# Performance work log

Measured on AMD Instinct MI355X. Metric: run time of the kernel, lower is better.

## Reference

```python
import jax, jax.numpy as jnp
import numpy as np

B, C, H, W = 4, 1024, 14, 14
L = 80          # num labels / graph nodes
WD = 300        # word embedding dim
INTER = 1024    # semantic intermediary dim
OUT = 2048      # output_dim
TIME_STEP = 3


def setup_inputs() -> dict:
    key = jax.random.key(0)
    ks = jax.random.split(key, 24)
    s = 0.02  # weight scale to keep gates/tanh in sane range
    return {
        "img_feature_map": jax.random.normal(ks[0], (B, C, H, W), jnp.float32),
        "word_embedding": jax.random.normal(ks[1], (L, WD), jnp.float32),
        "adjacency": jax.random.uniform(ks[2], (L, L), jnp.float32) / L,
        "fc1_w": jax.random.normal(ks[3], (INTER, C), jnp.float32) * s,
        "fc2_w": jax.random.normal(ks[4], (INTER, WD), jnp.float32) * s,
        "fc3_w": jax.random.normal(ks[5], (INTER, INTER), jnp.float32) * s,
        "fc3_b": jnp.zeros((INTER,), jnp.float32),
        "fca_w": jax.random.normal(ks[6], (1, INTER), jnp.float32) * s,
        "fca_b": jnp.zeros((1,), jnp.float32),
        "w3": jax.random.normal(ks[7], (C, 2 * C), jnp.float32) * s,
        "b3": jnp.zeros((C,), jnp.float32),
        "u3": jax.random.normal(ks[8], (C, C), jnp.float32) * s,
        "u3b": jnp.zeros((C,), jnp.float32),
        "w4": jax.random.normal(ks[9], (C, 2 * C), jnp.float32) * s,
        "b4": jnp.zeros((C,), jnp.float32),
        "w5": jax.random.normal(ks[10], (C, 2 * C), jnp.float32) * s,
        "b5": jnp.zeros((C,), jnp.float32),
        "u5": jax.random.normal(ks[11], (C, C), jnp.float32) * s,
        "u5b": jnp.zeros((C,), jnp.float32),
        "fco_w": jax.random.normal(ks[12], (OUT, 2 * C), jnp.float32) * s,
        "fco_b": jnp.zeros((OUT,), jnp.float32),
    }


def _semantic(fmap, word_emb, fc1_w, fc2_w, fc3_w, fc3_b, fca_w, fca_b):
    # Faithful to torch: view(-1, C) on a contiguous (B,C,H,W) tensor is a raw
    # row-major reinterpret (NOT a BHWC transpose). jnp.reshape matches.
    b, c, h, w = fmap.shape
    x = fmap.reshape(-1, c)                                   # (B*H*W, C)
    f_wh = x @ fc1_w.T                                        # (N, INTER)
    f_wd = word_emb @ fc2_w.T                                 # (L, INTER)
    lb = jnp.tanh(f_wh[:, None, :] * f_wd[None, :, :])        # (N, L, INTER)
    lb = lb @ fc3_w.T + fc3_b                                 # (N, L, INTER)
    coeff = lb @ fca_w.T + fca_b                              # (N, L, 1)
    coeff = coeff.reshape(b, L, h * w)                        # torch .view semantics
    coeff = jax.nn.softmax(coeff, axis=2)
    coeff = coeff.reshape(b, h, w, L)
    fmap_bhwc = fmap.reshape(b, h, w, c)                      # raw reinterpret, as torch
    return jnp.einsum('bhwl,bhwc->blc', coeff, fmap_bhwc)     # (B, L, C)


def _ggnn(nodes, adj, w3, b3, u3, u3b, w4, b4, w5, b5, u5, u5b):
    for _ in range(TIME_STEP):
        a = jnp.einsum('nm,bmd->bnd', adj, nodes)             # in == out matrix
        av = jnp.concatenate([a, a], axis=-1)                 # (B, L, 2C)
        u3x = nodes @ u3.T + u3b
        z = jax.nn.sigmoid(av @ w3.T + b3 + u3x)
        r = jax.nn.sigmoid(av @ w4.T + b4 + u3x)              # torch bug: reuses fc_eq3_u
        hcand = jnp.tanh(av @ w5.T + b5 + (r * nodes) @ u5.T + u5b)
        nodes = (1.0 - z) * nodes + z * hcand
    return nodes


def reference(img_feature_map, word_embedding, adjacency,
              fc1_w, fc2_w, fc3_w, fc3_b, fca_w, fca_b,
              w3, b3, u3, u3b, w4, b4, w5, b5, u5, u5b,
              fco_w, fco_b):
    g = _semantic(img_feature_map, word_embedding,
                  fc1_w, fc2_w, fc3_w, fc3_b, fca_w, fca_b)   # (B, L, C)
    nodes = _ggnn(g, adjacency, w3, b3, u3, u3b, w4, b4, w5, b5, u5, u5b)
    feat = jnp.concatenate([nodes, g], axis=-1)               # (B, L, 2C)
    out = jnp.tanh(feat @ fco_w.T + fco_b)                    # (B, L, OUT)
    return out
```

## Files before the change

kernel.cpp:

```cpp
#include <hip/hip_runtime.h>
#include <hip/hip_bf16.h>

#define LL 80
#define NPIX 784
#define PBATCH 15680

#define DI __device__ __forceinline__

typedef short s8v __attribute__((ext_vector_type(8)));
typedef short short4v __attribute__((ext_vector_type(4)));
typedef float f32x4 __attribute__((ext_vector_type(4)));

DI float b2f(__hip_bfloat16 x) { return __bfloat162float(x); }
DI float s2f(short h) { return __uint_as_float(((unsigned int)(unsigned short)h) << 16); }

DI short f2b(float x) {
    unsigned int b = __float_as_uint(x);
    b += 0x7fffu + ((b >> 16) & 1u);
    return (short)(b >> 16);
}

template <int F> DI float LD(const void* p, int i) {
    if (F) return ((const float*)p)[i];
    return b2f(((const __hip_bfloat16*)p)[i]);
}

DI float fast_tanh(float x) {
    float e = __expf(2.0f * x);
    return 1.0f - 2.0f / (e + 1.0f);
}
DI float fast_sigmoid(float x) { return 1.0f / (1.0f + __expf(-x)); }

__global__ __launch_bounds__(256) void detect_dtype(const void* probe, int n, int* flag) {
    __shared__ int bad;
    if (threadIdx.x == 0) bad = 0;
    __syncthreads();
    int c = 0;
    for (int i = threadIdx.x; i < n; i += 256) {
        float v = b2f(((const __hip_bfloat16*)probe)[i]);
        if (!(fabsf(v) < 1000.0f)) c++;
    }
    if (c) atomicAdd(&bad, c);
    __syncthreads();
    if (threadIdx.x == 0) *flag = (bad > 8) ? 1 : 0;
}

DI void cvt_part(int f, const void* src, short* __restrict__ dst, int blk, int n) {
    int i0 = (blk * 256 + threadIdx.x) * 4;
    if (i0 >= n) return;
    if (f) {
        float4 v = *(const float4*)((const float*)src + i0);
        short4v o = { f2b(v.x), f2b(v.y), f2b(v.z), f2b(v.w) };
        *(short4v*)(dst + i0) = o;
    } else {
        *(short4v*)(dst + i0) = *(const short4v*)((const short*)src + i0);
    }
}

DI void cvt_pad(int f, const void* src, short* __restrict__ dst, int blk, int n) {
    int i0 = (blk * 256 + threadIdx.x) * 4;
    if (i0 >= n) return;
    int row = i0 / 320;
    int k = i0 - row * 320;
    short4v o = {0, 0, 0, 0};
    if (k < 300) {
        if (f) {
            float4 v = *(const float4*)((const float*)src + row * 300 + k);
            o.x = f2b(v.x); o.y = f2b(v.y); o.z = f2b(v.z); o.w = f2b(v.w);
        } else {
            o = *(const short4v*)((const short*)src + row * 300 + k);
        }
    }
    *(short4v*)(dst + i0) = o;
}

DI void wcat_part(int f, const void* w3, const void* w4, const void* w5, const void* u3,
                  short* __restrict__ wcat, int blk) {
    int i0 = (blk * 256 + threadIdx.x) * 4;
    int nr = i0 >> 10, k = i0 & 1023;
    int j = nr >> 10, r = nr & 1023;
    const void* W = (j == 0) ? w3 : (j == 1) ? w4 : (j == 2) ? w5 : u3;
    float4 v;
    if (j < 3) {
        if (f) {
            float4 x = *(const float4*)((const float*)W + r * 2048 + k);
            float4 y = *(const float4*)((const float*)W + r * 2048 + 1024 + k);
            v.x = x.x + y.x; v.y = x.y + y.y; v.z = x.z + y.z; v.w = x.w + y.w;
        } else {
            const short* Ws = (const short*)W;
            short4v x = *(const short4v*)(Ws + r * 2048 + k);
            short4v y = *(const short4v*)(Ws + r * 2048 + 1024 + k);
            v.x = s2f(x.x) + s2f(y.x); v.y = s2f(x.y) + s2f(y.y);
            v.z = s2f(x.z) + s2f(y.z); v.w = s2f(x.w) + s2f(y.w);
        }
    } else {
        if (f) v = *(const float4*)((const float*)W + r * 1024 + k);
        else {
            short4v x = *(const short4v*)((const short*)W + r * 1024 + k);
            v.x = s2f(x.x); v.y = s2f(x.y); v.z = s2f(x.z); v.w = s2f(x.w);
        }
    }
    short4v o = { f2b(v.x), f2b(v.y), f2b(v.z), f2b(v.w) };
    *(short4v*)(wcat + i0) = o;
}

template <int F>
DI void prep_upart(const void* fc3_w, const void* fca_w,
                   float* __restrict__ u_part, int blk) {
    int kseg = blk >> 4, jseg = blk & 15;
    int k = kseg * 256 + threadIdx.x;
    int j0 = jseg * 64;
    float acc = 0.f;
    for (int j = j0; j < j0 + 64; j++)
        acc += LD<F>(fca_w, j) * LD<F>(fc3_w, j * 1024 + k);
    u_part[jseg * 1024 + k] = acc;
}

template <int F>
DI void prep_c0(const void* fc3_b, const void* fca_w, const void* fca_b,
                float* c0, float* red) {
    float acc = 0.f;
    for (int j = threadIdx.x; j < 1024; j += 256)
        acc += LD<F>(fc3_b, j) * LD<F>(fca_w, j);
    red[threadIdx.x] = acc;
    __syncthreads();
    for (int s = 128; s > 0; s >>= 1) {
        if (threadIdx.x < s) red[threadIdx.x] += red[threadIdx.x + s];
        __syncthreads();
    }
    if (threadIdx.x == 0) *c0 = red[0] + LD<F>(fca_b, 0);
}

__global__ __launch_bounds__(256) void mega_prep(
    const int* flag,
    const void* fmap, const void* fc1_w, const void* u5w,
    const void* w3, const void* w4, const void* w5, const void* u3,
    const void* fc3_w, const void* fc3_b, const void* fca_w, const void* fca_b,
    const void* word, const void* fc2_w,
    short* fmap_b, short* fc1w_b, short* u5w_b, short* wcat_b,
    short* word_b, short* fc2w_b,
    float* u_part, float* c0) {
    __shared__ float red[256];
    int f = *flag;
    int bid = blockIdx.x;
    if      (bid < 784)  cvt_part(f, fmap,  fmap_b, bid,        802816);
    else if (bid < 1808) cvt_part(f, fc1_w, fc1w_b, bid - 784,  1048576);
    else if (bid < 2832) cvt_part(f, u5w,   u5w_b,  bid - 1808, 1048576);
    else if (bid < 6928) wcat_part(f, w3, w4, w5, u3, wcat_b, bid - 2832);
    else if (bid < 6992) {
        if (f) prep_upart<1>(fc3_w, fca_w, u_part, bid - 6928);
        else   prep_upart<0>(fc3_w, fca_w, u_part, bid - 6928);
    } else if (bid == 6992) {
        if (f) prep_c0<1>(fc3_b, fca_w, fca_b, c0, red);
        else   prep_c0<0>(fc3_b, fca_w, fca_b, c0, red);
    }
    else if (bid < 7018) cvt_pad(f, word,  word_b, bid - 6993, 25600);
    else                 cvt_pad(f, fc2_w, fc2w_b, bid - 7018, 327680);
}

__global__ __launch_bounds__(256) void cvt_k(const int* flag, const void* src,
                                             short* __restrict__ dst, int n) {
    cvt_part(*flag, src, dst, blockIdx.x, n);
}

DI void mcore_b(const short* __restrict__ A, int lda,
                const short* __restrict__ B, int ldb,
                float* __restrict__ C, int ldc,
                int M, int kb, int ke, int m0, int n0) {
    __shared__ short As[4][64][8];
    __shared__ short Ws[4][64][8];
    const int tid = threadIdx.x;
    const int wv = tid >> 6, lane = tid & 63;
    const int mA = tid & 63, qA = tid >> 6;
    f32x4 acc[4] = {};

    for (int k0 = kb; k0 < ke; k0 += 32) {
        s8v va = {0,0,0,0,0,0,0,0};
        int gm = m0 + mA;
        if (gm < M) va = *(const s8v*)(A + gm * lda + k0 + 8 * qA);
        *(s8v*)&As[mA >> 4][(mA & 15) | (qA << 4)][0] = va;
        s8v vb = *(const s8v*)(B + (n0 + mA) * ldb + k0 + 8 * qA);
        *(s8v*)&Ws[mA >> 4][(mA & 15) | (qA << 4)][0] = vb;
        __syncthreads();
        s8v af = *(const s8v*)&As[wv][lane][0];
#pragma unroll
        for (int nf = 0; nf < 4; nf++) {
            s8v bf = *(const s8v*)&Ws[nf][lane][0];
            acc[nf] = __builtin_amdgcn_mfma_f32_16x16x32_bf16(af, bf, acc[nf], 0, 0, 0);
        }
        __syncthreads();
    }

    const int q = lane >> 4, cc = lane & 15;
#pragma unroll
    for (int nf = 0; nf < 4; nf++) {
        int n = n0 + 16 * nf + cc;
#pragma unroll
        for (int r = 0; r < 4; r++) {
            int m = m0 + 16 * wv + q * 4 + r;
            if (m < M) C[m * ldc + n] = acc[nf][r];
        }
    }
}

__global__ __launch_bounds__(256) void mfma_sem(
    const short* __restrict__ fmap_b, const short* __restrict__ fc1w_b,
    const short* __restrict__ word_b, const short* __restrict__ fc2w_b,
    const float* __restrict__ u_part, float* __restrict__ u,
    float* __restrict__ fhP, float* __restrict__ f_wd) {
    int bid = blockIdx.x;
    if (bid < 416) {
        int z = bid / 208, r = bid % 208;
        int by = r / 16, bx = r % 16;
        mcore_b(fmap_b, 1024, fc1w_b, 1024, fhP + z * 802816, 1024,
                NPIX, z * 512, z * 512 + 512, by * 64, bx * 64);
    } else if (bid < 448) {
        int r = bid - 416;
        int by = r >> 4, bx = r & 15;
        mcore_b(word_b, 320, fc2w_b, 320, f_wd, 1024,
                80, 0, 320, by * 64, bx * 64);
    } else {
        int k = (bid - 448) * 256 + threadIdx.x;
        float a = 0.f;
#pragma unroll
        for (int s = 0; s < 16; s++) a += u_part[s * 1024 + k];
        u[k] = a;
    }
}

__global__ __launch_bounds__(256) void mfma_gate(
    const short* __restrict__ a_b, const short* __restrict__ nodes_b,
    const short* __restrict__ wcat_b, float* __restrict__ gP) {
    int z = blockIdx.z;
    const short* A = (blockIdx.x >= 48) ? nodes_b : a_b;
    mcore_b(A, 1024, wcat_b, 1024, gP + z * 1310720, 4096,
            320, z * 512, z * 512 + 512, blockIdx.y * 64, blockIdx.x * 64);
}

__global__ __launch_bounds__(256) void mfma_u5(
    const short* __restrict__ rn_b, const short* __restrict__ u5w_b,
    float* __restrict__ u5P) {
    int z = blockIdx.z;
    mcore_b(rn_b, 1024, u5w_b, 1024, u5P + z * 327680, 1024,
            320, z * 256, z * 256 + 256, blockIdx.y * 64, blockIdx.x * 64);
}

__global__ __launch_bounds__(256) void mfma_fin(
    const short* __restrict__ nodes_b, const short* __restrict__ g_b,
    const short* __restrict__ fcow_b, float* __restrict__ finP) {
    int z = blockIdx.z;
    const short* A = z ? (g_b - 1024) : nodes_b;
    mcore_b(A, 1024, fcow_b, 2048, finP + z * 655360, 2048,
            320, z * 1024, z * 1024 + 1024, blockIdx.y * 64, blockIdx.x * 64);
}

__global__ void fin_combine(const int* flag, const float* __restrict__ finP,
                            const void* fco_b, void* out, int n) {
    int i4 = (blockIdx.x * 256 + threadIdx.x) * 4;
    if (i4 >= n) return;
    int c = i4 & 2047;
    float4 p0 = *(const float4*)(finP + i4);
    float4 p1 = *(const float4*)(finP + 655360 + i4);
    int f = *flag;
    float v0 = fast_tanh(p0.x + p1.x + (f ? LD<1>(fco_b, c)   : LD<0>(fco_b, c)));
    float v1 = fast_tanh(p0.y + p1.y + (f ? LD<1>(fco_b, c+1) : LD<0>(fco_b, c+1)));
    float v2 = fast_tanh(p0.z + p1.z + (f ? LD<1>(fco_b, c+2) : LD<0>(fco_b, c+2)));
    float v3 = fast_tanh(p0.w + p1.w + (f ? LD<1>(fco_b, c+3) : LD<0>(fco_b, c+3)));
    if (f) {
        float4 o = {v0, v1, v2, v3};
        *(float4*)((float*)out + i4) = o;
    } else {
        short4v o = { f2b(v0), f2b(v1), f2b(v2), f2b(v3) };
        *(short4v*)((short*)out + i4) = o;
    }
}

__global__ __launch_bounds__(256) void coeff_kernel(
    const float* __restrict__ fhP, const float* __restrict__ f_wd,
    const float* __restrict__ u, const float* __restrict__ c0p,
    float* __restrict__ s) {
    int n = blockIdx.x;
    __shared__ float4 fh4[256];
    __shared__ float4 uu4[256];
    int t = threadIdx.x;
    {
        float4 a0 = *(const float4*)(fhP + n * 1024 + t * 4);
        float4 a1 = *(const float4*)(fhP + 802816 + n * 1024 + t * 4);
        float4 fv = {a0.x + a1.x, a0.y + a1.y, a0.z + a1.z, a0.w + a1.w};
        fh4[t] = fv;
        uu4[t] = *(const float4*)(u + t * 4);
    }
    __syncthreads();
    float c0 = *c0p;
    int wave = t >> 6, lane = t & 63;
    int b = n / 196, hw = n % 196;
    int l0 = blockIdx.y * 40;
    for (int l = l0 + wave; l < l0 + 40; l += 4) {
        const float4* fd4 = (const float4*)(f_wd + l * 1024);
        float p = 0.f;
#pragma unroll
        for (int k = 0; k < 4; k++) {
            int idx = lane + k * 64;
            float4 h = fh4[idx];
            float4 d = fd4[idx];
            float4 uu = uu4[idx];
            p += fast_tanh(h.x * d.x) * uu.x;
            p += fast_tanh(h.y * d.y) * uu.y;
            p += fast_tanh(h.z * d.z) * uu.z;
            p += fast_tanh(h.w * d.w) * uu.w;
        }
        for (int off = 32; off > 0; off >>= 1) p += __shfl_down(p, off);
        if (lane == 0) s[b * PBATCH + hw * LL + l] = p + c0;
    }
}

__global__ __launch_bounds__(64) void softmax196(float* __restrict__ s) {
    float* p = s + blockIdx.x * 196;
    int lane = threadIdx.x;
    float v[4];
    float mx = -1e30f;
#pragma unroll
    for (int i = 0; i < 4; i++) {
        int idx = lane + i * 64;
        v[i] = (idx < 196) ? p[idx] : -1e30f;
        mx = fmaxf(mx, v[i]);
    }
    for (int off = 32; off > 0; off >>= 1) mx = fmaxf(mx, __shfl_down(mx, off));
    mx = __shfl(mx, 0);
    float sum = 0.f;
#pragma unroll
    for (int i = 0; i < 4; i++) {
        int idx = lane + i * 64;
        if (idx < 196) { v[i] = __expf(v[i] - mx); sum += v[i]; }
    }
    for (int off = 32; off > 0; off >>= 1) sum += __shfl_down(sum, off);
    sum = __shfl(sum, 0);
    float inv = 1.f / sum;
#pragma unroll
    for (int i = 0; i < 4; i++) {
        int idx = lane + i * 64;
        if (idx < 196) p[idx] = v[i] * inv;
    }
}

__global__ __launch_bounds__(256) void g_kernel(
    const float* __restrict__ s, const short* __restrict__ fmap_b,
    float* __restrict__ nodes, short* __restrict__ nodes_b, short* __restrict__ g_b) {
    int bl = blockIdx.x;
    int b = bl / LL, l = bl % LL;
    __shared__ float co[196];
    for (int i = threadIdx.x; i < 196; i += 256)
        co[i] = s[b * PBATCH + i * LL + l];
    __syncthreads();
    int c4 = threadIdx.x * 4;
    const short* base = fmap_b + b * 196 * 1024 + c4;
    float a0 = 0.f, a1 = 0.f, a2 = 0.f, a3 = 0.f;
    for (int hw = 0; hw < 196; hw++) {
        short4v v = *(const short4v*)(base + hw * 1024);
        float w = co[hw];
        a0 += w * s2f(v.x); a1 += w * s2f(v.y);
        a2 += w * s2f(v.z); a3 += w * s2f(v.w);
    }
    int o = bl * 1024 + c4;
    float4 fa = {a0, a1, a2, a3};
    *(float4*)(nodes + o) = fa;
    short4v bb = { f2b(a0), f2b(a1), f2b(a2), f2b(a3) };
    *(short4v*)(nodes_b + o) = bb;
    *(short4v*)(g_b + o) = bb;
}

template <int F>
DI void adj_core(float* arw, const void* adj, const float* nodes, short* a_b) {
    int bl = blockIdx.x;
    int b = bl / LL, l = bl % LL;
    if (threadIdx.x < LL) arw[threadIdx.x] = LD<F>(adj, l * LL + threadIdx.x);
    __syncthreads();
    int c4 = threadIdx.x * 4;
    const float* nb = nodes + b * LL * 1024 + c4;
    float a0 = 0.f, a1 = 0.f, a2 = 0.f, a3 = 0.f;
    for (int m = 0; m < LL; m++) {
        float am = arw[m];
        float4 nd = *(const float4*)(nb + m * 1024);
        a0 += am * nd.x; a1 += am * nd.y; a2 += am * nd.z; a3 += am * nd.w;
    }
    short4v bb = { f2b(a0), f2b(a1), f2b(a2), f2b(a3) };
    *(short4v*)(a_b + bl * 1024 + c4) = bb;
}

__global__ __launch_bounds__(256) void adj_kernel(
    const int* flag, const void* adj, const float* nodes, short* a_b) {
    __shared__ float arw[LL];
    if (*flag) adj_core<1>(arw, adj, nodes, a_b);
    else       adj_core<0>(arw, adj, nodes, a_b);
}

template <int F>
DI void ew_r_core(const float* gP, const float* nodes,
                  const void* b4, const void* u3b, short* rn_b, int i4) {
    int m = i4 >> 10, c = i4 & 1023;
    int base = m * 4096;
    float4 r0 = *(const float4*)(gP + base + 1024 + c);
    float4 r1 = *(const float4*)(gP + 1310720 + base + 1024 + c);
    float4 x0 = *(const float4*)(gP + base + 3072 + c);
    float4 x1 = *(const float4*)(gP + 1310720 + base + 3072 + c);
    float4 nd = *(const float4*)(nodes + i4);
    short4v o;
    o.x = f2b(fast_sigmoid(r0.x + r1.x + x0.x + x1.x + LD<F>(b4, c)   + LD<F>(u3b, c))   * nd.x);
    o.y = f2b(fast_sigmoid(r0.y + r1.y + x0.y + x1.y + LD<F>(b4, c+1) + LD<F>(u3b, c+1)) * nd.y);
    o.z = f2b(fast_sigmoid(r0.z + r1.z + x0.z + x1.z + LD<F>(b4, c+2) + LD<F>(u3b, c+2)) * nd.z);
    o.w = f2b(fast_sigmoid(r0.w + r1.w + x0.w + x1.w + LD<F>(b4, c+3) + LD<F>(u3b, c+3)) * nd.w);
    *(short4v*)(rn_b + i4) = o;
}

__global__ void ew_r(const int* flag, const float* gP, const float* nodes,
                     const void* b4, const void* u3b, short* rn_b, int n) {
    int i4 = (blockIdx.x * 256 + threadIdx.x) * 4;
    if (i4 >= n) return;
    if (*flag) ew_r_core<1>(gP, nodes, b4, u3b, rn_b, i4);
    else       ew_r_core<0>(gP, nodes, b4, u3b, rn_b, i4);
}

template <int F>
DI void ewu(const float* gP, const float* u5P,
            const void* b3, const void* u3b, const void* b5, const void* u5b,
            float* nodes, short* nodes_b, int i4) {
    int m = i4 >> 10, c = i4 & 1023;
    int base = m * 4096;
    float4 z0 = *(const float4*)(gP + base + c);
    float4 z1 = *(const float4*)(gP + 1310720 + base + c);
    float4 h0 = *(const float4*)(gP + base + 2048 + c);
    float4 h1 = *(const float4*)(gP + 1310720 + base + 2048 + c);
    float4 x0 = *(const float4*)(gP + base + 3072 + c);
    float4 x1 = *(const float4*)(gP + 1310720 + base + 3072 + c);
    float4 u0 = *(const float4*)(u5P + i4);
    float4 u1 = *(const float4*)(u5P + 327680 + i4);
    float4 u2 = *(const float4*)(u5P + 655360 + i4);
    float4 u3v = *(const float4*)(u5P + 983040 + i4);
    float4 nd = *(const float4*)(nodes + i4);
    float4 out;
#define EWU1(CH, CO) { \
    float z = fast_sigmoid(z0.CH + z1.CH + x0.CH + x1.CH + LD<F>(b3, c+CO) + LD<F>(u3b, c+CO)); \
    float h = fast_tanh(h0.CH + h1.CH + u0.CH + u1.CH + u2.CH + u3v.CH + LD<F>(b5, c+CO) + LD<F>(u5b, c+CO)); \
    out.CH = (1.f - z) * nd.CH + z * h; }
    EWU1(x, 0) EWU1(y, 1) EWU1(z, 2) EWU1(w, 3)
#undef EWU1
    *(float4*)(nodes + i4) = out;
    short4v bb = { f2b(out.x), f2b(out.y), f2b(out.z), f2b(out.w) };
    *(short4v*)(nodes_b + i4) = bb;
}

__global__ void ew_upd(const int* flag, const float* gP, const float* u5P,
                       const void* b3, const void* u3b, const void* b5, const void* u5b,
                       float* nodes, short* nodes_b, int n) {
    int i4 = (blockIdx.x * 256 + threadIdx.x) * 4;
    if (i4 >= n) return;
    if (*flag) ewu<1>(gP, u5P, b3, u3b, b5, u5b, nodes, nodes_b, i4);
    else       ewu<0>(gP, u5P, b3, u3b, b5, u5b, nodes, nodes_b, i4);
}

extern "C" void kernel_launch(void* const* d_in, const int* in_sizes, int n_in,
                              void* d_out, int out_size, void* d_ws, size_t ws_size,
                              hipStream_t stream) {
    const void* fmap  = d_in[0];
    const void* word  = d_in[1];
    const void* adjm  = d_in[2];
    const void* fc1_w = d_in[3];
    const void* fc2_w = d_in[4];
    const void* fc3_w = d_in[5];
    const void* fc3_b = d_in[6];
    const void* fca_w = d_in[7];
    const void* fca_b = d_in[8];
    const void* w3    = d_in[9];
    const void* b3    = d_in[10];
    const void* u3    = d_in[11];
    const void* u3b   = d_in[12];
    const void* w4    = d_in[13];
    const void* b4    = d_in[14];
    const void* w5    = d_in[15];
    const void* b5    = d_in[16];
    const void* u5    = d_in[17];
    const void* u5b   = d_in[18];
    const void* fco_w = d_in[19];
    const void* fco_b = d_in[20];

    int*   flag    = (int*)d_ws;
    float* P       = (float*)d_ws + 16;
    float* nodes   = P;                       P += 327680;
    short* nodes_b = (short*)P;               P += 163840;
    short* g_b     = (short*)P;               P += 163840;
    short* a_b     = (short*)P;               P += 163840;
    short* rn_b    = (short*)P;               P += 163840;
    short* u5w_b   = (short*)P;               P += 524288;
    short* wcat_b  = (short*)P;               P += 2097152;
    float* R       = P;
    float* fhP    = R;
    float* f_wd   = R + 1605632;
    float* u_part = f_wd + 81920;
    float* u      = u_part + 16384;
    float* c0     = u + 1024;
    float* s      = c0 + 16;
    short* fmap_b = (short*)(s + 62720);
    short* fc1w_b = fmap_b + 802816;
    short* word_b = fc1w_b + 1048576;
    short* fc2w_b = word_b + 25600;
    float* gP     = R;
    float* u5P    = R + 2621440;
    float* finP   = R;
    short* fcow_b = (short*)(R + 1310720);

    detect_dtype<<<1, 256, 0, stream>>>(fc1_w, 4096, flag);

    mega_prep<<<7338, 256, 0, stream>>>(flag, fmap, fc1_w, u5,
                                        w3, w4, w5, u3,
                                        fc3_w, fc3_b, fca_w, fca_b,
                                        word, fc2_w,
                                        fmap_b, fc1w_b, u5w_b, wcat_b,
                                        word_b, fc2w_b, u_part, c0);

    mfma_sem<<<452, 256, 0, stream>>>(fmap_b, fc1w_b, word_b, fc2w_b,
                                      u_part, u, fhP, f_wd);
    coeff_kernel<<<dim3(NPIX, 2), 256, 0, stream>>>(fhP, f_wd, u, c0, s);
    softmax196<<<320, 64, 0, stream>>>(s);
    g_kernel<<<320, 256, 0, stream>>>(s, fmap_b, nodes, nodes_b, g_b);

    for (int t = 0; t < 3; t++) {
        adj_kernel<<<320, 256, 0, stream>>>(flag, adjm, nodes, a_b);
        mfma_gate<<<dim3(64, 5, 2), 256, 0, stream>>>(a_b, nodes_b, wcat_b, gP);
        ew_r<<<320, 256, 0, stream>>>(flag, gP, nodes, b4, u3b, rn_b, 327680);
        mfma_u5<<<dim3(16, 5, 4), 256, 0, stream>>>(rn_b, u5w_b, u5P);
        ew_upd<<<320, 256, 0, stream>>>(flag, gP, u5P, b3, u3b, b5, u5b,
                                        nodes, nodes_b, 327680);
    }

    cvt_k<<<4096, 256, 0, stream>>>(flag, fco_w, fcow_b, 4194304);
    mfma_fin<<<dim3(32, 5, 2), 256, 0, stream>>>(nodes_b, g_b, fcow_b, finP);
    fin_combine<<<640, 256, 0, stream>>>(flag, finP, fco_b, d_out, 655360);
}
```

Measured before the change: 359.5 us.

## Rewrite tanh via exp2/rcp identity and block four pixels per coeff block

```diff
diff --git a/kernel.cpp b/kernel.cpp
--- a/kernel.cpp
+++ b/kernel.cpp
@@ -128,7 +128,11 @@
         if (threadIdx.x < s) red[threadIdx.x] += red[threadIdx.x + s];
         __syncthreads();
     }
-    if (threadIdx.x == 0) *c0 = red[0] + LD<F>(fca_b, 0);
+    if (threadIdx.x == 0) {
+        float v = red[0] + LD<F>(fca_b, 0);
+        c0[0] = v;
+        c0[1] = v;
+    }
 }
 
 __global__ __launch_bounds__(256) void mega_prep(
@@ -206,7 +210,7 @@
 __global__ __launch_bounds__(256) void mfma_sem(
     const short* __restrict__ fmap_b, const short* __restrict__ fc1w_b,
     const short* __restrict__ word_b, const short* __restrict__ fc2w_b,
-    const float* __restrict__ u_part, float* __restrict__ u,
+    const float* __restrict__ u_part, float* __restrict__ u, float* __restrict__ c0,
     float* __restrict__ fhP, float* __restrict__ f_wd) {
     int bid = blockIdx.x;
     if (bid < 416) {
@@ -220,11 +224,19 @@
         mcore_b(word_b, 320, fc2w_b, 320, f_wd, 1024,
                 80, 0, 320, by * 64, bx * 64);
     } else {
+        __shared__ float red[256];
         int k = (bid - 448) * 256 + threadIdx.x;
         float a = 0.f;
 #pragma unroll
-        for (int s = 0; s < 16; s++) a += u_part[s * 1024 + k];
+        for (int si = 0; si < 16; si++) a += u_part[si * 1024 + k];
         u[k] = a;
+        red[threadIdx.x] = a;
+        __syncthreads();
+        for (int st = 128; st > 0; st >>= 1) {
+            if (threadIdx.x < st) red[threadIdx.x] += red[threadIdx.x + st];
+            __syncthreads();
+        }
+        if (threadIdx.x == 0) atomicAdd(c0 + 1, red[0]);
     }
 }
 
@@ -279,38 +291,59 @@
     const float* __restrict__ fhP, const float* __restrict__ f_wd,
     const float* __restrict__ u, const float* __restrict__ c0p,
     float* __restrict__ s) {
-    int n = blockIdx.x;
-    __shared__ float4 fh4[256];
-    __shared__ float4 uu4[256];
+    __shared__ float h2s[4][1024];
+    __shared__ float us[1024];
+    const float K2 = 2.8853900817779268f;
     int t = threadIdx.x;
-    {
+    int n0 = blockIdx.x * 4;
+#pragma unroll
+    for (int r = 0; r < 4; r++) {
+        int n = n0 + r;
         float4 a0 = *(const float4*)(fhP + n * 1024 + t * 4);
         float4 a1 = *(const float4*)(fhP + 802816 + n * 1024 + t * 4);
-        float4 fv = {a0.x + a1.x, a0.y + a1.y, a0.z + a1.z, a0.w + a1.w};
-        fh4[t] = fv;
-        uu4[t] = *(const float4*)(u + t * 4);
-    }
+        float4 hv = {K2 * (a0.x + a1.x), K2 * (a0.y + a1.y),
+                     K2 * (a0.z + a1.z), K2 * (a0.w + a1.w)};
+        *(float4*)&h2s[r][t * 4] = hv;
+    }
+    *(float4*)&us[t * 4] = *(const float4*)(u + t * 4);
     __syncthreads();
-    float c0 = *c0p;
+    float c0U = c0p[1];
     int wave = t >> 6, lane = t & 63;
-    int b = n / 196, hw = n % 196;
-    int l0 = blockIdx.y * 40;
-    for (int l = l0 + wave; l < l0 + 40; l += 4) {
+    int b = n0 / 196, hw0 = n0 % 196;
+    int l0 = blockIdx.y * 20;
+    for (int l = l0 + wave; l < l0 + 20; l += 4) {
         const float4* fd4 = (const float4*)(f_wd + l * 1024);
-        float p = 0.f;
-#pragma unroll
-        for (int k = 0; k < 4; k++) {
-            int idx = lane + k * 64;
-            float4 h = fh4[idx];
-            float4 d = fd4[idx];
-            float4 uu = uu4[idx];
-            p += fast_tanh(h.x * d.x) * uu.x;
-            p += fast_tanh(h.y * d.y) * uu.y;
-            p += fast_tanh(h.z * d.z) * uu.z;
-            p += fast_tanh(h.w * d.w) * uu.w;
-        }
-        for (int off = 32; off > 0; off >>= 1) p += __shfl_down(p, off);
-        if (lane == 0) s[b * PBATCH + hw * LL + l] = p + c0;
+        float p0 = 0.f, p1 = 0.f, p2 = 0.f, p3 = 0.f;
+#pragma unroll
+        for (int j = 0; j < 4; j++) {
+            int idx = lane + j * 64;
+            float4 d  = fd4[idx];
+            float4 uu = *(const float4*)&us[idx * 4];
+            float4 h0 = *(const float4*)&h2s[0][idx * 4];
+            float4 h1 = *(const float4*)&h2s[1][idx * 4];
+            float4 h2 = *(const float4*)&h2s[2][idx * 4];
+            float4 h3 = *(const float4*)&h2s[3][idx * 4];
+#define TERM(P, H) \
+    P += uu.x * __builtin_amdgcn_rcpf(1.0f + __builtin_amdgcn_exp2f(H.x * d.x)); \
+    P += uu.y * __builtin_amdgcn_rcpf(1.0f + __builtin_amdgcn_exp2f(H.y * d.y)); \
+    P += uu.z * __builtin_amdgcn_rcpf(1.0f + __builtin_amdgcn_exp2f(H.z * d.z)); \
+    P += uu.w * __builtin_amdgcn_rcpf(1.0f + __builtin_amdgcn_exp2f(H.w * d.w));
+            TERM(p0, h0) TERM(p1, h1) TERM(p2, h2) TERM(p3, h3)
+#undef TERM
+        }
+        for (int off = 32; off > 0; off >>= 1) {
+            p0 += __shfl_down(p0, off);
+            p1 += __shfl_down(p1, off);
+            p2 += __shfl_down(p2, off);
+            p3 += __shfl_down(p3, off);
+        }
+        if (lane == 0) {
+            float* sp = s + b * PBATCH + hw0 * LL + l;
+            sp[0]      = c0U - 2.f * p0;
+            sp[LL]     = c0U - 2.f * p1;
+            sp[2 * LL] = c0U - 2.f * p2;
+            sp[3 * LL] = c0U - 2.f * p3;
+        }
     }
 }
 
@@ -518,8 +551,8 @@
                                         word_b, fc2w_b, u_part, c0);
 
     mfma_sem<<<452, 256, 0, stream>>>(fmap_b, fc1w_b, word_b, fc2w_b,
-                                      u_part, u, fhP, f_wd);
-    coeff_kernel<<<dim3(NPIX, 2), 256, 0, stream>>>(fhP, f_wd, u, c0, s);
+                                      u_part, u, c0, fhP, f_wd);
+    coeff_kernel<<<dim3(196, 4), 256, 0, stream>>>(fhP, f_wd, u, c0, s);
     softmax196<<<320, 64, 0, stream>>>(s);
     g_kernel<<<320, 256, 0, stream>>>(s, fmap_b, nodes, nodes_b, g_b);
 
```

Result: faster. 341.2 us (-5.1%).
